# Performance work log

Measured on AMD Instinct MI355X. Metric: run time of the kernel, lower is better.

The kernel has to match this reference:

```python
import jax, jax.numpy as jnp
import numpy as np

N_NODES = 100000
N_EDGES = 1600000
IN_C, HID_C, OUT_C = 128, 128, 64


def gcn_conv(x, W, b, src, dst, n_nodes):
    """PyG-style GCNConv: h = x @ W; add self-loops; symmetric deg^-1/2 norm;
    scatter-add aggregation; + bias. Self-loop contribution added analytically
    (norm for self-loop edge i->i is deg_i^-1) instead of materializing edges."""
    h = x @ W  # [N, C_out]
    # degree over dst including self-loops (edge weights are all ones)
    deg = jax.ops.segment_sum(jnp.ones((src.shape[0],), h.dtype), dst,
                              num_segments=n_nodes) + 1.0
    dinv = jax.lax.rsqrt(deg)  # deg >= 1 always
    norm = dinv[src] * dinv[dst]  # [E]
    agg = jax.ops.segment_sum(h[src] * norm[:, None], dst, num_segments=n_nodes)
    agg = agg + h * (dinv * dinv)[:, None]  # self-loop term
    return agg + b


def setup_inputs() -> dict:
    key = jax.random.key(0)
    k0, k1, k2, k3, k4, k5 = jax.random.split(key, 6)
    x = jax.random.normal(k0, (N_NODES, IN_C), dtype=jnp.float32)
    edge_index = jax.random.randint(k1, (2, N_EDGES), 0, N_NODES, dtype=jnp.int64)
    s1 = 1.0 / np.sqrt(IN_C)
    s2 = 1.0 / np.sqrt(HID_C)
    W1 = jax.random.uniform(k2, (IN_C, HID_C), jnp.float32, -s1, s1)
    b1 = jax.random.uniform(k3, (HID_C,), jnp.float32, -s1, s1)
    W2 = jax.random.uniform(k4, (HID_C, OUT_C), jnp.float32, -s2, s2)
    b2 = jax.random.uniform(k5, (OUT_C,), jnp.float32, -s2, s2)
    return {"x": x, "W1": W1, "b1": b1, "W2": W2, "b2": b2,
            "edge_index": edge_index}


def reference(x, W1, b1, W2, b2, edge_index):
    src, dst = edge_index[0], edge_index[1]
    h = gcn_conv(x, W1, b1, src, dst, N_NODES)
    h = jax.nn.relu(h)
    out = gcn_conv(h, W2, b2, src, dst, N_NODES)
    return out
```

## Files before the change

### kernel.cpp

```cpp
#include <hip/hip_runtime.h>


static constexpr int BSHIFT = 7;
static constexpr int BWIDTH = 1 << BSHIFT;
static constexpr int MAXBUCK = 2048;
static constexpr int NPART = 256;

static constexpr size_t OFF_FLAG = 0;
static constexpr size_t OFF_DEG  = 256;
static constexpr size_t OFF_ROW  = 458752;
static constexpr size_t OFF_BSUM = 917504;
static constexpr size_t OFF_CCNT = 925696;
static constexpr size_t OFF_COFF = 937984;
static constexpr size_t OFF_DINV = 962560;
static constexpr size_t OFF_CSR  = 1376256;
static constexpr size_t OFF_HS1  = 8388608;
static constexpr size_t OFF_OUT1 = 35651584;
static constexpr size_t OFF_HS2  = 62914560;
static constexpr size_t OFF_H2   = 75714560;
static constexpr size_t OFF_W1S  = 77811712;
static constexpr size_t OFF_W2S  = 77844480;

__device__ __forceinline__ unsigned short f2bf(float f) {
    unsigned u = __float_as_uint(f);
    u += 0x7fffu + ((u >> 16) & 1u);
    return (unsigned short)(u >> 16);
}

typedef __attribute__((ext_vector_type(8))) short bf16x8;
typedef __attribute__((ext_vector_type(4))) float f32x4;

__global__ void detect_kernel(const unsigned* __restrict__ w,
                              unsigned* __restrict__ flag,
                              unsigned* __restrict__ ccnt, int nbuck) {
    int i = blockIdx.x * blockDim.x + threadIdx.x;
    if (i <= nbuck) ccnt[i] = 0;
    if (w[2 * i + 1] != 0u) atomicOr(flag, 1u);
}

__device__ __forceinline__ int edge_dst(const unsigned* w, unsigned flag,
                                        int e, int E) {
    return flag ? (int)w[E + e] : (int)w[2 * E + 2 * e];
}
__device__ __forceinline__ int edge_src(const unsigned* w, unsigned flag,
                                        int e, int E) {
    return flag ? (int)w[e] : (int)w[2 * e];
}

__global__ __launch_bounds__(1024) void coarse_hist_kernel(
    const unsigned* __restrict__ w, const unsigned* __restrict__ flag,
    unsigned* __restrict__ ccnt, unsigned* __restrict__ h2, int E, int nbuck) {
    __shared__ unsigned hist[MAXBUCK];
    for (int i = threadIdx.x; i < nbuck; i += 1024) hist[i] = 0;
    __syncthreads();
    const unsigned f = *flag;
    const int per = (E + gridDim.x - 1) / gridDim.x;
    const int e0 = blockIdx.x * per, e1 = min(E, e0 + per);
    for (int e = e0 + (int)threadIdx.x; e < e1; e += 1024)
        atomicAdd(&hist[edge_dst(w, f, e, E) >> BSHIFT], 1u);
    __syncthreads();
    for (int i = threadIdx.x; i < nbuck; i += 1024) {
        unsigned h = hist[i];
        h2[(size_t)i * NPART + blockIdx.x] = h;
        if (h) atomicAdd(&ccnt[i], h);
    }
}

__global__ __launch_bounds__(1024) void coarse_scan_kernel(
    const unsigned* __restrict__ ccnt, unsigned* __restrict__ coff, int nbuck) {
    __shared__ unsigned sh[1024];
    const int t = threadIdx.x;
    unsigned run = 0;
    for (int b0 = 0; b0 < nbuck; b0 += 1024) {
        unsigned v = (b0 + t < nbuck) ? ccnt[b0 + t] : 0u;
        sh[t] = v;
        __syncthreads();
        for (int off = 1; off < 1024; off <<= 1) {
            unsigned a = (t >= off) ? sh[t - off] : 0u;
            __syncthreads();
            sh[t] += a;
            __syncthreads();
        }
        if (b0 + t < nbuck) coff[b0 + t] = run + sh[t] - v;
        run += sh[1023];
        __syncthreads();
    }
    if (t == 0) coff[nbuck] = run;
}

__global__ __launch_bounds__(NPART) void off2d_kernel(
    unsigned* __restrict__ h2, const unsigned* __restrict__ coff) {
    __shared__ unsigned sh[NPART];
    const int b = blockIdx.x, t = threadIdx.x;
    unsigned v = h2[(size_t)b * NPART + t];
    sh[t] = v;
    __syncthreads();
#pragma unroll
    for (int off = 1; off < NPART; off <<= 1) {
        unsigned a = (t >= off) ? sh[t - off] : 0u;
        __syncthreads();
        sh[t] += a;
        __syncthreads();
    }
    h2[(size_t)b * NPART + t] = coff[b] + sh[t] - v;
}

__global__ __launch_bounds__(1024) void partition_kernel(
    const unsigned* __restrict__ w, const unsigned* __restrict__ flag,
    const unsigned* __restrict__ h2, unsigned* __restrict__ part, int E,
    int nbuck) {
    __shared__ unsigned lcur[MAXBUCK];
    for (int i = threadIdx.x; i < nbuck; i += 1024)
        lcur[i] = h2[(size_t)i * NPART + blockIdx.x];
    __syncthreads();
    const unsigned f = *flag;
    const int per = (E + gridDim.x - 1) / gridDim.x;
    const int e0 = blockIdx.x * per, e1 = min(E, e0 + per);
    for (int e = e0 + (int)threadIdx.x; e < e1; e += 1024) {
        int d = edge_dst(w, f, e, E);
        int s = edge_src(w, f, e, E);
        unsigned pos = atomicAdd(&lcur[d >> BSHIFT], 1u);
        part[pos] = (unsigned)s | ((unsigned)(d & (BWIDTH - 1)) << 20);
    }
}

__global__ __launch_bounds__(256) void bucket_csr_kernel(
    const unsigned* __restrict__ part, const unsigned* __restrict__ coff,
    unsigned* __restrict__ deg, int* __restrict__ csr, int N) {
    __shared__ unsigned cnt[BWIDTH];
    __shared__ unsigned sc[BWIDTH];
    __shared__ unsigned cur[BWIDTH];
    const int b = blockIdx.x, base = b << BSHIFT, t = threadIdx.x;
    if (t < BWIDTH) cnt[t] = 0;
    __syncthreads();
    const int e0 = (int)coff[b], e1 = (int)coff[b + 1];
    for (int e = e0 + t; e < e1; e += 256)
        atomicAdd(&cnt[part[e] >> 20], 1u);
    __syncthreads();
    if (t < BWIDTH && base + t < N) deg[base + t] = cnt[t];
    if (t < BWIDTH) sc[t] = cnt[t];
    __syncthreads();
#pragma unroll
    for (int off = 1; off < BWIDTH; off <<= 1) {
        unsigned a = (t < BWIDTH && t >= off) ? sc[t - off] : 0u;
        __syncthreads();
        if (t < BWIDTH) sc[t] += a;
        __syncthreads();
    }
    if (t < BWIDTH) cur[t] = (unsigned)e0 + sc[t] - cnt[t];
    __syncthreads();
    for (int e = e0 + t; e < e1; e += 256) {
        unsigned pk = part[e];
        unsigned p = atomicAdd(&cur[pk >> 20], 1u);
        csr[p] = (int)(pk & 0xFFFFFu);
    }
}

__global__ __launch_bounds__(1024) void scan1_kernel(
    const unsigned* __restrict__ deg, unsigned* __restrict__ row,
    unsigned* __restrict__ bsum, int N) {
    __shared__ unsigned sh[1024];
    int gid = blockIdx.x * 1024 + threadIdx.x;
    int t = threadIdx.x;
    unsigned v = (gid < N) ? deg[gid] : 0u;
    sh[t] = v;
    __syncthreads();
#pragma unroll
    for (int off = 1; off < 1024; off <<= 1) {
        unsigned add = (t >= off) ? sh[t - off] : 0u;
        __syncthreads();
        sh[t] += add;
        __syncthreads();
    }
    if (gid < N) row[gid + 1] = sh[t];
    if (t == 1023) bsum[blockIdx.x] = sh[1023];
}

__global__ __launch_bounds__(1024) void scan2_kernel(unsigned* __restrict__ bsum,
                                                     int NB) {
    __shared__ unsigned sh[1024];
    const int t = threadIdx.x;
    unsigned v = (t < NB) ? bsum[t] : 0u;
    sh[t] = v;
    __syncthreads();
#pragma unroll
    for (int off = 1; off < 1024; off <<= 1) {
        unsigned a = (t >= off) ? sh[t - off] : 0u;
        __syncthreads();
        sh[t] += a;
        __syncthreads();
    }
    if (t < NB) bsum[t] = sh[t] - v;
}

__global__ void scan3_kernel(unsigned* __restrict__ row,
                             const unsigned* __restrict__ bsum,
                             const unsigned* __restrict__ deg,
                             float* __restrict__ dinv, int N) {
    int gid = blockIdx.x * blockDim.x + threadIdx.x;
    if (gid >= N) return;
    row[gid + 1] += bsum[gid >> 10];
    if (gid == 0) row[0] = 0u;
    dinv[gid] = rsqrtf((float)deg[gid] + 1.0f);
}

__global__ __launch_bounds__(256) void wprep_kernel(
    const float* __restrict__ W1, const float* __restrict__ W2,
    unsigned short* __restrict__ O1, unsigned short* __restrict__ O2) {
    const float* W = blockIdx.x ? W2 : W1;
    unsigned short* O = blockIdx.x ? O2 : O1;
    const int BN = blockIdx.x ? 64 : 128;
    const int total = 128 * BN / 4;
    for (int g = threadIdx.x; g < total; g += 256) {
        int n = g % BN, k0 = (g / BN) * 4;
        ushort4 u;
        u.x = f2bf(W[(size_t)(k0 + 0) * BN + n]);
        u.y = f2bf(W[(size_t)(k0 + 1) * BN + n]);
        u.z = f2bf(W[(size_t)(k0 + 2) * BN + n]);
        u.w = f2bf(W[(size_t)(k0 + 3) * BN + n]);
        int off = ((((n >> 4) * 4 + (k0 >> 5)) * 16 + (n & 15)) * 4 +
                   ((k0 >> 3) & 3)) * 8 + (k0 & 4);
        *(ushort4*)(O + off) = u;
    }
}

template <int BN, bool ABF16>
__global__ __launch_bounds__(256) void gemm_mfma(
    const void* __restrict__ Av, const unsigned short* __restrict__ Bs,
    const float* __restrict__ dinv, unsigned short* __restrict__ out, int M) {
    constexpr int NT = BN / 16;
    const int t = threadIdx.x;
    const int row0 = blockIdx.x * 128;
    const int w = t >> 6, lane = t & 63;
    const int m = lane & 15, q = lane >> 4;
    const int fb = (m * 4 + q) * 8;

    const int r0 = row0 + (2 * w) * 16 + m;
    const int r1 = r0 + 16;

    f32x4 acc[2][NT];
#pragma unroll
    for (int lt = 0; lt < 2; lt++)
#pragma unroll
        for (int nt = 0; nt < NT; nt++) acc[lt][nt] = (f32x4){0.f, 0.f, 0.f, 0.f};

#pragma unroll
    for (int ks = 0; ks < 4; ks++) {
        const int k0 = ks * 32 + q * 8;
        bf16x8 a0 = (bf16x8){0, 0, 0, 0, 0, 0, 0, 0};
        bf16x8 a1 = (bf16x8){0, 0, 0, 0, 0, 0, 0, 0};
        if (ABF16) {
            const unsigned short* A = (const unsigned short*)Av;
            if (r0 < M) a0 = *(const bf16x8*)(A + (size_t)r0 * 128 + k0);
            if (r1 < M) a1 = *(const bf16x8*)(A + (size_t)r1 * 128 + k0);
        } else {
            const float* A = (const float*)Av;
            if (r0 < M) {
                const float* p = A + (size_t)r0 * 128 + k0;
                f32x4 lo = *(const f32x4*)p, hi = *(const f32x4*)(p + 4);
                a0[0] = (short)f2bf(lo[0]); a0[1] = (short)f2bf(lo[1]);
                a0[2] = (short)f2bf(lo[2]); a0[3] = (short)f2bf(lo[3]);
                a0[4] = (short)f2bf(hi[0]); a0[5] = (short)f2bf(hi[1]);
                a0[6] = (short)f2bf(hi[2]); a0[7] = (short)f2bf(hi[3]);
            }
            if (r1 < M) {
                const float* p = A + (size_t)r1 * 128 + k0;
                f32x4 lo = *(const f32x4*)p, hi = *(const f32x4*)(p + 4);
                a1[0] = (short)f2bf(lo[0]); a1[1] = (short)f2bf(lo[1]);
                a1[2] = (short)f2bf(lo[2]); a1[3] = (short)f2bf(lo[3]);
                a1[4] = (short)f2bf(hi[0]); a1[5] = (short)f2bf(hi[1]);
                a1[6] = (short)f2bf(hi[2]); a1[7] = (short)f2bf(hi[3]);
            }
        }
#pragma unroll
        for (int nt = 0; nt < NT; nt++) {
            bf16x8 b = *(const bf16x8*)(Bs + (nt * 4 + ks) * 512 + fb);
            acc[0][nt] = __builtin_amdgcn_mfma_f32_16x16x32_bf16(a0, b, acc[0][nt], 0, 0, 0);
            acc[1][nt] = __builtin_amdgcn_mfma_f32_16x16x32_bf16(a1, b, acc[1][nt], 0, 0, 0);
        }
    }

#pragma unroll
    for (int lt = 0; lt < 2; lt++) {
#pragma unroll
        for (int r = 0; r < 4; r++) {
            int row = row0 + w * 32 + lt * 16 + q * 4 + r;
            if (row < M) {
                float s = dinv[row];
#pragma unroll
                for (int nt = 0; nt < NT; nt++)
                    out[(size_t)row * BN + nt * 16 + m] = f2bf(acc[lt][nt][r] * s);
            }
        }
    }
}

template <int C, bool RELU, bool OUTBF>
__global__ __launch_bounds__(256) void agg_kernel(
    const int* __restrict__ csr, const unsigned* __restrict__ row,
    const unsigned short* __restrict__ hsb, const float* __restrict__ dinv,
    const float* __restrict__ bias, void* __restrict__ outv, int N) {
    constexpr int LPN = C / 8;
    const int tid = blockIdx.x * 256 + threadIdx.x;
    const int i = tid / LPN;
    const int l = tid % LPN;
    if (i >= N) return;

    const int co = 8 * l;
    float s0 = 0.f, s1 = 0.f, s2 = 0.f, s3 = 0.f,
          s4 = 0.f, s5 = 0.f, s6 = 0.f, s7 = 0.f;
    {
        uint4 u = *(const uint4*)(hsb + (size_t)i * C + co);
        s0 += __uint_as_float(u.x << 16); s1 += __uint_as_float(u.x & 0xffff0000u);
        s2 += __uint_as_float(u.y << 16); s3 += __uint_as_float(u.y & 0xffff0000u);
        s4 += __uint_as_float(u.z << 16); s5 += __uint_as_float(u.z & 0xffff0000u);
        s6 += __uint_as_float(u.w << 16); s7 += __uint_as_float(u.w & 0xffff0000u);
    }

    const int rs = (int)row[i], re = (int)row[i + 1];
    for (int e0 = rs; e0 < re; e0 += LPN) {
        int idx = (e0 + l < re) ? csr[e0 + l] : 0;
        const int cnt = min(LPN, re - e0);
#pragma unroll 4
        for (int j = 0; j < cnt; j++) {
            int s = __shfl(idx, j, LPN);
            uint4 u = *(const uint4*)(hsb + (size_t)s * C + co);
            s0 += __uint_as_float(u.x << 16); s1 += __uint_as_float(u.x & 0xffff0000u);
            s2 += __uint_as_float(u.y << 16); s3 += __uint_as_float(u.y & 0xffff0000u);
            s4 += __uint_as_float(u.z << 16); s5 += __uint_as_float(u.z & 0xffff0000u);
            s6 += __uint_as_float(u.w << 16); s7 += __uint_as_float(u.w & 0xffff0000u);
        }
    }

    const float sc = dinv[i];
    const float4 ba = *(const float4*)(bias + co);
    const float4 bb = *(const float4*)(bias + co + 4);
    float o0 = s0 * sc + ba.x, o1 = s1 * sc + ba.y;
    float o2 = s2 * sc + ba.z, o3 = s3 * sc + ba.w;
    float o4 = s4 * sc + bb.x, o5 = s5 * sc + bb.y;
    float o6 = s6 * sc + bb.z, o7 = s7 * sc + bb.w;
    if (RELU) {
        o0 = fmaxf(o0, 0.f); o1 = fmaxf(o1, 0.f); o2 = fmaxf(o2, 0.f);
        o3 = fmaxf(o3, 0.f); o4 = fmaxf(o4, 0.f); o5 = fmaxf(o5, 0.f);
        o6 = fmaxf(o6, 0.f); o7 = fmaxf(o7, 0.f);
    }
    if (OUTBF) {
        uint4 u;
        u.x = (unsigned)f2bf(o0) | ((unsigned)f2bf(o1) << 16);
        u.y = (unsigned)f2bf(o2) | ((unsigned)f2bf(o3) << 16);
        u.z = (unsigned)f2bf(o4) | ((unsigned)f2bf(o5) << 16);
        u.w = (unsigned)f2bf(o6) | ((unsigned)f2bf(o7) << 16);
        *(uint4*)((unsigned short*)outv + (size_t)i * C + co) = u;
    } else {
        float4 a = make_float4(o0, o1, o2, o3);
        float4 b = make_float4(o4, o5, o6, o7);
        *(float4*)((float*)outv + (size_t)i * C + co) = a;
        *(float4*)((float*)outv + (size_t)i * C + co + 4) = b;
    }
}

extern "C" void kernel_launch(void* const* d_in, const int* in_sizes, int n_in,
                              void* d_out, int out_size, void* d_ws,
                              size_t ws_size, hipStream_t stream) {
    const float* x  = (const float*)d_in[0];
    const float* W1 = (const float*)d_in[1];
    const float* b1 = (const float*)d_in[2];
    const float* W2 = (const float*)d_in[3];
    const float* b2 = (const float*)d_in[4];
    const unsigned* ew = (const unsigned*)d_in[5];
    const int E = in_sizes[5] / 2;
    const int N = in_sizes[0] / 128;
    const int NB = (N + 1023) >> 10;
    const int nbuck = (N + BWIDTH - 1) >> BSHIFT;

    char* ws = (char*)d_ws;
    unsigned* flag = (unsigned*)(ws + OFF_FLAG);
    unsigned* deg  = (unsigned*)(ws + OFF_DEG);
    unsigned* row  = (unsigned*)(ws + OFF_ROW);
    unsigned* bsum = (unsigned*)(ws + OFF_BSUM);
    unsigned* ccnt = (unsigned*)(ws + OFF_CCNT);
    unsigned* coff = (unsigned*)(ws + OFF_COFF);
    float* dinv    = (float*)(ws + OFF_DINV);
    int* csr       = (int*)(ws + OFF_CSR);
    unsigned short* hs1  = (unsigned short*)(ws + OFF_HS1);
    unsigned short* out1 = (unsigned short*)(ws + OFF_OUT1);
    unsigned short* hs2  = (unsigned short*)(ws + OFF_HS2);
    unsigned* h2   = (unsigned*)(ws + OFF_H2);
    unsigned short* w1s  = (unsigned short*)(ws + OFF_W1S);
    unsigned short* w2s  = (unsigned short*)(ws + OFF_W2S);
    unsigned* part = (unsigned*)(ws + OFF_HS1);

    hipMemsetAsync(flag, 0, 4, stream);

    wprep_kernel<<<2, 256, 0, stream>>>(W1, W2, w1s, w2s);

    detect_kernel<<<16, 256, 0, stream>>>(ew, flag, ccnt, nbuck);
    coarse_hist_kernel<<<NPART, 1024, 0, stream>>>(ew, flag, ccnt, h2, E, nbuck);
    coarse_scan_kernel<<<1, 1024, 0, stream>>>(ccnt, coff, nbuck);
    off2d_kernel<<<nbuck, NPART, 0, stream>>>(h2, coff);
    partition_kernel<<<NPART, 1024, 0, stream>>>(ew, flag, h2, part, E, nbuck);
    bucket_csr_kernel<<<nbuck, 256, 0, stream>>>(part, coff, deg, csr, N);
    scan1_kernel<<<NB, 1024, 0, stream>>>(deg, row, bsum, N);
    scan2_kernel<<<1, 1024, 0, stream>>>(bsum, NB);
    scan3_kernel<<<(N + 255) / 256, 256, 0, stream>>>(row, bsum, deg, dinv, N);

    gemm_mfma<128, false><<<(N + 127) / 128, 256, 0, stream>>>(x, w1s, dinv, hs1, N);
    agg_kernel<128, true, true><<<(N * 16 + 255) / 256, 256, 0, stream>>>(
        csr, row, hs1, dinv, b1, out1, N);

    gemm_mfma<64, true><<<(N + 127) / 128, 256, 0, stream>>>(out1, w2s, dinv, hs2, N);
    agg_kernel<64, false, false><<<(N * 8 + 255) / 256, 256, 0, stream>>>(
        csr, row, hs2, dinv, b2, d_out, N);
}
```

Baseline: 305.7 us.

## Fuse CSR build kernels to cut launches and drop separate scan passes

```diff
diff --git a/kernel.cpp b/kernel.cpp
--- a/kernel.cpp
+++ b/kernel.cpp
@@ -6,10 +6,7 @@
 static constexpr int MAXBUCK = 2048;
 static constexpr int NPART = 256;
 
-static constexpr size_t OFF_FLAG = 0;
-static constexpr size_t OFF_DEG  = 256;
 static constexpr size_t OFF_ROW  = 458752;
-static constexpr size_t OFF_BSUM = 917504;
 static constexpr size_t OFF_CCNT = 925696;
 static constexpr size_t OFF_COFF = 937984;
 static constexpr size_t OFF_DINV = 962560;
@@ -30,12 +27,11 @@
 typedef __attribute__((ext_vector_type(8))) short bf16x8;
 typedef __attribute__((ext_vector_type(4))) float f32x4;
 
-__global__ void detect_kernel(const unsigned* __restrict__ w,
-                              unsigned* __restrict__ flag,
-                              unsigned* __restrict__ ccnt, int nbuck) {
-    int i = blockIdx.x * blockDim.x + threadIdx.x;
-    if (i <= nbuck) ccnt[i] = 0;
-    if (w[2 * i + 1] != 0u) atomicOr(flag, 1u);
+__device__ __forceinline__ unsigned detect_flag(const unsigned* __restrict__ w) {
+    unsigned fl = 0;
+#pragma unroll
+    for (int k = 1; k < 32; k += 2) fl |= w[k];
+    return fl;
 }
 
 __device__ __forceinline__ int edge_dst(const unsigned* w, unsigned flag,
@@ -47,14 +43,35 @@
     return flag ? (int)w[e] : (int)w[2 * e];
 }
 
-__global__ __launch_bounds__(1024) void coarse_hist_kernel(
-    const unsigned* __restrict__ w, const unsigned* __restrict__ flag,
-    unsigned* __restrict__ ccnt, unsigned* __restrict__ h2, int E, int nbuck) {
+__global__ __launch_bounds__(1024) void hist_wprep_kernel(
+    const unsigned* __restrict__ w, unsigned* __restrict__ ccnt,
+    unsigned* __restrict__ h2, int E, int nbuck,
+    const float* __restrict__ W1, const float* __restrict__ W2,
+    unsigned short* __restrict__ O1, unsigned short* __restrict__ O2) {
+    if (blockIdx.x >= NPART) {
+        const int which = blockIdx.x - NPART;
+        const float* W = which ? W2 : W1;
+        unsigned short* O = which ? O2 : O1;
+        const int BN = which ? 64 : 128;
+        const int total = 128 * BN / 4;
+        for (int g = threadIdx.x; g < total; g += 1024) {
+            int n = g % BN, k0 = (g / BN) * 4;
+            ushort4 u;
+            u.x = f2bf(W[(size_t)(k0 + 0) * BN + n]);
+            u.y = f2bf(W[(size_t)(k0 + 1) * BN + n]);
+            u.z = f2bf(W[(size_t)(k0 + 2) * BN + n]);
+            u.w = f2bf(W[(size_t)(k0 + 3) * BN + n]);
+            int off = ((((n >> 4) * 4 + (k0 >> 5)) * 16 + (n & 15)) * 4 +
+                       ((k0 >> 3) & 3)) * 8 + (k0 & 4);
+            *(ushort4*)(O + off) = u;
+        }
+        return;
+    }
     __shared__ unsigned hist[MAXBUCK];
     for (int i = threadIdx.x; i < nbuck; i += 1024) hist[i] = 0;
     __syncthreads();
-    const unsigned f = *flag;
-    const int per = (E + gridDim.x - 1) / gridDim.x;
+    const unsigned f = detect_flag(w);
+    const int per = (E + NPART - 1) / NPART;
     const int e0 = blockIdx.x * per, e1 = min(E, e0 + per);
     for (int e = e0 + (int)threadIdx.x; e < e1; e += 1024)
         atomicAdd(&hist[edge_dst(w, f, e, E) >> BSHIFT], 1u);
@@ -66,32 +83,26 @@
     }
 }
 
-__global__ __launch_bounds__(1024) void coarse_scan_kernel(
-    const unsigned* __restrict__ ccnt, unsigned* __restrict__ coff, int nbuck) {
-    __shared__ unsigned sh[1024];
-    const int t = threadIdx.x;
-    unsigned run = 0;
-    for (int b0 = 0; b0 < nbuck; b0 += 1024) {
-        unsigned v = (b0 + t < nbuck) ? ccnt[b0 + t] : 0u;
-        sh[t] = v;
-        __syncthreads();
-        for (int off = 1; off < 1024; off <<= 1) {
-            unsigned a = (t >= off) ? sh[t - off] : 0u;
-            __syncthreads();
-            sh[t] += a;
-            __syncthreads();
-        }
-        if (b0 + t < nbuck) coff[b0 + t] = run + sh[t] - v;
-        run += sh[1023];
-        __syncthreads();
-    }
-    if (t == 0) coff[nbuck] = run;
-}
-
-__global__ __launch_bounds__(NPART) void off2d_kernel(
-    unsigned* __restrict__ h2, const unsigned* __restrict__ coff) {
+__global__ __launch_bounds__(NPART) void scanoff_kernel(
+    const unsigned* __restrict__ ccnt, unsigned* __restrict__ coff,
+    unsigned* __restrict__ h2, int nbuck) {
+    __shared__ unsigned red[NPART];
     __shared__ unsigned sh[NPART];
     const int b = blockIdx.x, t = threadIdx.x;
+    unsigned p = 0;
+    for (int i = t; i < b; i += NPART) p += ccnt[i];
+    red[t] = p;
+    __syncthreads();
+#pragma unroll
+    for (int off = NPART / 2; off > 0; off >>= 1) {
+        if (t < off) red[t] += red[t + off];
+        __syncthreads();
+    }
+    const unsigned coffb = red[0];
+    if (t == 0) {
+        coff[b] = coffb;
+        if (b == nbuck - 1) coff[nbuck] = coffb + ccnt[b];
+    }
     unsigned v = h2[(size_t)b * NPART + t];
     sh[t] = v;
     __syncthreads();
@@ -102,19 +113,18 @@
         sh[t] += a;
         __syncthreads();
     }
-    h2[(size_t)b * NPART + t] = coff[b] + sh[t] - v;
+    h2[(size_t)b * NPART + t] = coffb + sh[t] - v;
 }
 
 __global__ __launch_bounds__(1024) void partition_kernel(
-    const unsigned* __restrict__ w, const unsigned* __restrict__ flag,
-    const unsigned* __restrict__ h2, unsigned* __restrict__ part, int E,
-    int nbuck) {
+    const unsigned* __restrict__ w, const unsigned* __restrict__ h2,
+    unsigned* __restrict__ part, int E, int nbuck) {
     __shared__ unsigned lcur[MAXBUCK];
     for (int i = threadIdx.x; i < nbuck; i += 1024)
         lcur[i] = h2[(size_t)i * NPART + blockIdx.x];
     __syncthreads();
-    const unsigned f = *flag;
-    const int per = (E + gridDim.x - 1) / gridDim.x;
+    const unsigned f = detect_flag(w);
+    const int per = (E + NPART - 1) / NPART;
     const int e0 = blockIdx.x * per, e1 = min(E, e0 + per);
     for (int e = e0 + (int)threadIdx.x; e < e1; e += 1024) {
         int d = edge_dst(w, f, e, E);
@@ -126,7 +136,8 @@
 
 __global__ __launch_bounds__(256) void bucket_csr_kernel(
     const unsigned* __restrict__ part, const unsigned* __restrict__ coff,
-    unsigned* __restrict__ deg, int* __restrict__ csr, int N) {
+    unsigned* __restrict__ row, float* __restrict__ dinv,
+    int* __restrict__ csr, int N) {
     __shared__ unsigned cnt[BWIDTH];
     __shared__ unsigned sc[BWIDTH];
     __shared__ unsigned cur[BWIDTH];
@@ -137,7 +148,6 @@
     for (int e = e0 + t; e < e1; e += 256)
         atomicAdd(&cnt[part[e] >> 20], 1u);
     __syncthreads();
-    if (t < BWIDTH && base + t < N) deg[base + t] = cnt[t];
     if (t < BWIDTH) sc[t] = cnt[t];
     __syncthreads();
 #pragma unroll
@@ -147,80 +157,20 @@
         if (t < BWIDTH) sc[t] += a;
         __syncthreads();
     }
-    if (t < BWIDTH) cur[t] = (unsigned)e0 + sc[t] - cnt[t];
+    if (t < BWIDTH) {
+        unsigned r = (unsigned)e0 + sc[t] - cnt[t];
+        cur[t] = r;
+        if (base + t < N) {
+            row[base + t] = r;
+            dinv[base + t] = rsqrtf((float)cnt[t] + 1.0f);
+        }
+    }
+    if (t == 0 && b == (int)gridDim.x - 1) row[N] = (unsigned)e1;
     __syncthreads();
     for (int e = e0 + t; e < e1; e += 256) {
         unsigned pk = part[e];
         unsigned p = atomicAdd(&cur[pk >> 20], 1u);
         csr[p] = (int)(pk & 0xFFFFFu);
-    }
-}
-
-__global__ __launch_bounds__(1024) void scan1_kernel(
-    const unsigned* __restrict__ deg, unsigned* __restrict__ row,
-    unsigned* __restrict__ bsum, int N) {
-    __shared__ unsigned sh[1024];
-    int gid = blockIdx.x * 1024 + threadIdx.x;
-    int t = threadIdx.x;
-    unsigned v = (gid < N) ? deg[gid] : 0u;
-    sh[t] = v;
-    __syncthreads();
-#pragma unroll
-    for (int off = 1; off < 1024; off <<= 1) {
-        unsigned add = (t >= off) ? sh[t - off] : 0u;
-        __syncthreads();
-        sh[t] += add;
-        __syncthreads();
-    }
-    if (gid < N) row[gid + 1] = sh[t];
-    if (t == 1023) bsum[blockIdx.x] = sh[1023];
-}
-
-__global__ __launch_bounds__(1024) void scan2_kernel(unsigned* __restrict__ bsum,
-                                                     int NB) {
-    __shared__ unsigned sh[1024];
-    const int t = threadIdx.x;
-    unsigned v = (t < NB) ? bsum[t] : 0u;
-    sh[t] = v;
-    __syncthreads();
-#pragma unroll
-    for (int off = 1; off < 1024; off <<= 1) {
-        unsigned a = (t >= off) ? sh[t - off] : 0u;
-        __syncthreads();
-        sh[t] += a;
-        __syncthreads();
-    }
-    if (t < NB) bsum[t] = sh[t] - v;
-}
-
-__global__ void scan3_kernel(unsigned* __restrict__ row,
-                             const unsigned* __restrict__ bsum,
-                             const unsigned* __restrict__ deg,
-                             float* __restrict__ dinv, int N) {
-    int gid = blockIdx.x * blockDim.x + threadIdx.x;
-    if (gid >= N) return;
-    row[gid + 1] += bsum[gid >> 10];
-    if (gid == 0) row[0] = 0u;
-    dinv[gid] = rsqrtf((float)deg[gid] + 1.0f);
-}
-
-__global__ __launch_bounds__(256) void wprep_kernel(
-    const float* __restrict__ W1, const float* __restrict__ W2,
-    unsigned short* __restrict__ O1, unsigned short* __restrict__ O2) {
-    const float* W = blockIdx.x ? W2 : W1;
-    unsigned short* O = blockIdx.x ? O2 : O1;
-    const int BN = blockIdx.x ? 64 : 128;
-    const int total = 128 * BN / 4;
-    for (int g = threadIdx.x; g < total; g += 256) {
-        int n = g % BN, k0 = (g / BN) * 4;
-        ushort4 u;
-        u.x = f2bf(W[(size_t)(k0 + 0) * BN + n]);
-        u.y = f2bf(W[(size_t)(k0 + 1) * BN + n]);
-        u.z = f2bf(W[(size_t)(k0 + 2) * BN + n]);
-        u.w = f2bf(W[(size_t)(k0 + 3) * BN + n]);
-        int off = ((((n >> 4) * 4 + (k0 >> 5)) * 16 + (n & 15)) * 4 +
-                   ((k0 >> 3) & 3)) * 8 + (k0 & 4);
-        *(ushort4*)(O + off) = u;
     }
 }
 
@@ -370,14 +320,10 @@
     const unsigned* ew = (const unsigned*)d_in[5];
     const int E = in_sizes[5] / 2;
     const int N = in_sizes[0] / 128;
-    const int NB = (N + 1023) >> 10;
     const int nbuck = (N + BWIDTH - 1) >> BSHIFT;
 
     char* ws = (char*)d_ws;
-    unsigned* flag = (unsigned*)(ws + OFF_FLAG);
-    unsigned* deg  = (unsigned*)(ws + OFF_DEG);
     unsigned* row  = (unsigned*)(ws + OFF_ROW);
-    unsigned* bsum = (unsigned*)(ws + OFF_BSUM);
     unsigned* ccnt = (unsigned*)(ws + OFF_CCNT);
     unsigned* coff = (unsigned*)(ws + OFF_COFF);
     float* dinv    = (float*)(ws + OFF_DINV);
@@ -390,19 +336,13 @@
     unsigned short* w2s  = (unsigned short*)(ws + OFF_W2S);
     unsigned* part = (unsigned*)(ws + OFF_HS1);
 
-    hipMemsetAsync(flag, 0, 4, stream);
-
-    wprep_kernel<<<2, 256, 0, stream>>>(W1, W2, w1s, w2s);
-
-    detect_kernel<<<16, 256, 0, stream>>>(ew, flag, ccnt, nbuck);
-    coarse_hist_kernel<<<NPART, 1024, 0, stream>>>(ew, flag, ccnt, h2, E, nbuck);
-    coarse_scan_kernel<<<1, 1024, 0, stream>>>(ccnt, coff, nbuck);
-    off2d_kernel<<<nbuck, NPART, 0, stream>>>(h2, coff);
-    partition_kernel<<<NPART, 1024, 0, stream>>>(ew, flag, h2, part, E, nbuck);
-    bucket_csr_kernel<<<nbuck, 256, 0, stream>>>(part, coff, deg, csr, N);
-    scan1_kernel<<<NB, 1024, 0, stream>>>(deg, row, bsum, N);
-    scan2_kernel<<<1, 1024, 0, stream>>>(bsum, NB);
-    scan3_kernel<<<(N + 255) / 256, 256, 0, stream>>>(row, bsum, deg, dinv, N);
+    hipMemsetAsync(ccnt, 0, (size_t)(nbuck + 1) * 4, stream);
+
+    hist_wprep_kernel<<<NPART + 2, 1024, 0, stream>>>(ew, ccnt, h2, E, nbuck,
+                                                      W1, W2, w1s, w2s);
+    scanoff_kernel<<<nbuck, NPART, 0, stream>>>(ccnt, coff, h2, nbuck);
+    partition_kernel<<<NPART, 1024, 0, stream>>>(ew, h2, part, E, nbuck);
+    bucket_csr_kernel<<<nbuck, 256, 0, stream>>>(part, coff, row, dinv, csr, N);
 
     gemm_mfma<128, false><<<(N + 127) / 128, 256, 0, stream>>>(x, w1s, dinv, hs1, N);
     agg_kernel<128, true, true><<<(N * 16 + 255) / 256, 256, 0, stream>>>(
```

New measurement: 278.9 us. 1.1x faster.
